# Performance work log

Hardware: AMD Instinct MI355X
Metric: run time of the kernel (lower is better)

The kernel has to match this reference:

```python
import jax, jax.numpy as jnp
import numpy as np
import math

D_MODEL, N_HEADS, D_HEAD, D_MLP = 768, 12, 64, 3072
LN_EPS = 1e-5
INIT_STD = 0.02


def gelu_new(x):
    # GPT-2 'new' gelu: 0.5*x*(1+tanh(sqrt(2/pi)*(x+0.044715*x^3)))
    c = math.sqrt(2.0 / math.pi)
    return 0.5 * x * (1.0 + jnp.tanh(c * (x + 0.044715 * jnp.power(x, 3.0))))


def layer_norm(x, w, b):
    mu = jnp.mean(x, axis=-1, keepdims=True)
    xc = x - mu
    scale = jnp.sqrt(jnp.mean(xc * xc, axis=-1, keepdims=True) + LN_EPS)
    return (xc / scale) * w + b


def setup_inputs() -> dict:
    key = jax.random.key(0)
    ks = jax.random.split(key, 8)
    resid_pre = jax.random.normal(ks[0], (8, 1024, D_MODEL), dtype=jnp.float32)
    W_Q = jax.random.normal(ks[1], (N_HEADS, D_MODEL, D_HEAD), dtype=jnp.float32) * INIT_STD
    W_K = jax.random.normal(ks[2], (N_HEADS, D_MODEL, D_HEAD), dtype=jnp.float32) * INIT_STD
    W_V = jax.random.normal(ks[3], (N_HEADS, D_MODEL, D_HEAD), dtype=jnp.float32) * INIT_STD
    W_O = jax.random.normal(ks[4], (N_HEADS, D_HEAD, D_MODEL), dtype=jnp.float32) * INIT_STD
    W_in = jax.random.normal(ks[5], (D_MODEL, D_MLP), dtype=jnp.float32) * INIT_STD
    W_out = jax.random.normal(ks[6], (D_MLP, D_MODEL), dtype=jnp.float32) * INIT_STD
    return {
        'resid_pre': resid_pre,
        'ln1_w': jnp.ones((D_MODEL,), jnp.float32), 'ln1_b': jnp.zeros((D_MODEL,), jnp.float32),
        'W_Q': W_Q, 'b_Q': jnp.zeros((N_HEADS, D_HEAD), jnp.float32),
        'W_K': W_K, 'b_K': jnp.zeros((N_HEADS, D_HEAD), jnp.float32),
        'W_V': W_V, 'b_V': jnp.zeros((N_HEADS, D_HEAD), jnp.float32),
        'W_O': W_O, 'b_O': jnp.zeros((D_MODEL,), jnp.float32),
        'ln2_w': jnp.ones((D_MODEL,), jnp.float32), 'ln2_b': jnp.zeros((D_MODEL,), jnp.float32),
        'W_in': W_in, 'b_in': jnp.zeros((D_MLP,), jnp.float32),
        'W_out': W_out, 'b_out': jnp.zeros((D_MODEL,), jnp.float32),
    }


def attention(x, W_Q, b_Q, W_K, b_K, W_V, b_V, W_O, b_O):
    # x: [b, s, d_model]
    q = jnp.einsum('bsd,hde->bshe', x, W_Q) + b_Q
    k = jnp.einsum('bsd,hde->bshe', x, W_K) + b_K
    v = jnp.einsum('bsd,hde->bshe', x, W_V) + b_V
    scores = jnp.einsum('bqhe,bkhe->bhqk', q, k) / math.sqrt(D_HEAD)
    s = x.shape[1]
    causal = jnp.triu(jnp.ones((s, s), dtype=bool), k=1)
    scores = jnp.where(causal, -jnp.inf, scores)
    pattern = jax.nn.softmax(scores, axis=-1)
    pattern = jnp.where(jnp.isnan(pattern), 0.0, pattern)
    z = jnp.einsum('bhqk,bkhe->bqhe', pattern, v)
    # per-head projection then sum over heads; b_O/n_heads per head sums to b_O
    return jnp.einsum('bqhe,hed->bqd', z, W_O) + b_O


def reference(resid_pre, ln1_w, ln1_b, W_Q, b_Q, W_K, b_K, W_V, b_V, W_O, b_O,
              ln2_w, ln2_b, W_in, b_in, W_out, b_out):
    normed1 = layer_norm(resid_pre, ln1_w, ln1_b)
    attn_out = attention(normed1, W_Q, b_Q, W_K, b_K, W_V, b_V, W_O, b_O)
    residual = resid_pre + attn_out
    normed2 = layer_norm(residual, ln2_w, ln2_b)
    pre = jnp.einsum('bsd,dm->bsm', normed2, W_in) + b_in
    mlp_out = jnp.einsum('bsm,md->bsd', gelu_new(pre), W_out) + b_out
    return residual + mlp_out
```

## Files before the change

kernel.cpp:

```cpp
#include <hip/hip_runtime.h>
#include <hip/hip_bf16.h>
#include <stdint.h>
#include <math.h>

typedef __bf16 bf16x8 __attribute__((ext_vector_type(8)));
typedef float f32x4 __attribute__((ext_vector_type(4)));
using bf16 = __hip_bfloat16;

__device__ inline float bf2f(bf16 x) { return __bfloat162float(x); }
__device__ inline bf16 f2bf(float x) { return __float2bfloat16(x); }

__device__ inline f32x4 mfma16(bf16x8 a, bf16x8 b, f32x4 c) {
  return __builtin_amdgcn_mfma_f32_16x16x32_bf16(a, b, c, 0, 0, 0);
}

__device__ inline void async16(const bf16* g, bf16* l) {
  __builtin_amdgcn_global_load_lds(
      (const __attribute__((address_space(1))) unsigned int*)g,
      (__attribute__((address_space(3))) unsigned int*)l, 16, 0, 0);
}

__device__ inline float gelu_new(float x) {
  float u2 = 1.5957691216057308f * (x + 0.044715f * x * x * x);
  float e = __expf(u2);
  float t = 1.0f - 2.0f * __builtin_amdgcn_rcpf(e + 1.0f);
  return 0.5f * x * (1.0f + t);
}

__device__ inline void ln_body(const float* __restrict__ x, const float* __restrict__ w,
                               const float* __restrict__ bb, bf16* __restrict__ out,
                               int row, int t, float* red) {
  size_t base = (size_t)row * 768;
  float v0 = x[base + t];
  float v1 = x[base + t + 256];
  float v2 = x[base + t + 512];
  float s = v0 + v1 + v2;
  float ss = v0 * v0 + v1 * v1 + v2 * v2;
#pragma unroll
  for (int off = 32; off > 0; off >>= 1) {
    s += __shfl_down(s, off, 64);
    ss += __shfl_down(ss, off, 64);
  }
  int wv = t >> 6, ln = t & 63;
  if (ln == 0) { red[wv] = s; red[4 + wv] = ss; }
  __syncthreads();
  s = red[0] + red[1] + red[2] + red[3];
  ss = red[4] + red[5] + red[6] + red[7];
  float mu = s * (1.0f / 768.0f);
  float var = ss * (1.0f / 768.0f) - mu * mu;
  float rinv = rsqrtf(var + 1e-5f);
  out[base + t]       = f2bf((v0 - mu) * rinv * w[t]       + bb[t]);
  out[base + t + 256] = f2bf((v1 - mu) * rinv * w[t + 256] + bb[t + 256]);
  out[base + t + 512] = f2bf((v2 - mu) * rinv * w[t + 512] + bb[t + 512]);
}

__global__ __launch_bounds__(256) void ln_kernel(const float* __restrict__ x,
                                                 const float* __restrict__ w,
                                                 const float* __restrict__ bb,
                                                 bf16* __restrict__ out) {
  __shared__ float red[8];
  ln_body(x, w, bb, out, blockIdx.x, threadIdx.x, red);
}

__device__ inline void transpose_body(const float* __restrict__ in, bf16* __restrict__ out,
                                      int R, int C, int bx, int by, int t,
                                      float (*tile)[33]) {
  int tx = t & 31, ty = t >> 5;
  int r0 = bx * 32, c0 = by * 32;
#pragma unroll
  for (int j = 0; j < 32; j += 8)
    tile[ty + j][tx] = in[(size_t)(r0 + ty + j) * C + c0 + tx];
  __syncthreads();
#pragma unroll
  for (int j = 0; j < 32; j += 8)
    out[(size_t)(c0 + ty + j) * R + r0 + tx] = f2bf(tile[tx][ty + j]);
}

__global__ __launch_bounds__(256) void prep_all(
    const float* __restrict__ resid_pre, const float* __restrict__ ln1_w,
    const float* __restrict__ ln1_b, bf16* __restrict__ n1,
    const float* __restrict__ Wq, const float* __restrict__ Wk,
    const float* __restrict__ Wv, bf16* __restrict__ Wqkv_t,
    const float* __restrict__ W_O, bf16* __restrict__ Wo_t,
    const float* __restrict__ W_in, bf16* __restrict__ Win_t,
    const float* __restrict__ W_out, bf16* __restrict__ Wout_t,
    const float* __restrict__ bq, const float* __restrict__ bk,
    const float* __restrict__ bv, float* __restrict__ bias_qkv) {
  __shared__ float tile[32][33];
  const int t = threadIdx.x;
  int bid = blockIdx.x;
  if (bid < 8192) {
    ln_body(resid_pre, ln1_w, ln1_b, n1, bid, t, &tile[0][0]);
    return;
  }
  bid -= 8192;
  if (bid < 1728) {
    int z = bid / 48, r = bid - z * 48;
    int which = z / 12, h = z - which * 12;
    const float* W = (which == 0) ? Wq : ((which == 1) ? Wk : Wv);
    transpose_body(W + (size_t)h * 768 * 64,
                   Wqkv_t + (size_t)which * 589824 + (size_t)h * 64 * 768,
                   768, 64, r % 24, r / 24, t, tile);
    return;
  }
  bid -= 1728;
  if (bid < 576) {
    transpose_body(W_O, Wo_t, 768, 768, bid % 24, bid / 24, t, tile);
    return;
  }
  bid -= 576;
  if (bid < 2304) {
    transpose_body(W_in, Win_t, 768, 3072, bid % 24, bid / 24, t, tile);
    return;
  }
  bid -= 2304;
  if (bid < 2304) {
    transpose_body(W_out, Wout_t, 3072, 768, bid % 96, bid / 96, t, tile);
    return;
  }
  bid -= 2304;
  int i = bid * 256 + t;
  if (i < 2304)
    bias_qkv[i] = (i < 768) ? bq[i] : ((i < 1536) ? bk[i - 768] : bv[i - 1536]);
}

enum { MODE_QKV = 0, MODE_ADDF = 2, MODE_GELU = 3 };

template <int MODE, int MROWS>
__global__ __launch_bounds__(256) void gemm_bt(
    const bf16* __restrict__ A, const bf16* __restrict__ BT,
    const float* __restrict__ bias,
    const float* __restrict__ addend,
    float* __restrict__ out_f32,
    bf16* __restrict__ out_bf16,
    int M, int N, int K) {
  constexpr int MI = MROWS / 32;
  __shared__ __align__(16) bf16 smem[(MROWS + 128) * 64];
  bf16* Alds = smem;
  bf16* Blds = smem + MROWS * 64;
  const int t = threadIdx.x;
  const int wave = t >> 6, lane = t & 63;
  const int lm = lane & 15, quad = lane >> 4;
  const int wm = wave >> 1, wn = wave & 1;
  const int m0 = blockIdx.x * MROWS, n0 = blockIdx.y * 128;

  f32x4 acc[MI][4] = {};

  for (int k0 = 0; k0 < K; k0 += 64) {
#pragma unroll
    for (int i = 0; i < MI; i++) {
      int c = i * 256 + t;
      int r = c >> 3, cs = c & 7;
      async16(A + (size_t)(m0 + r) * K + k0 + ((cs ^ (r & 7)) << 3), &Alds[c * 8]);
    }
#pragma unroll
    for (int i = 0; i < 4; i++) {
      int c = i * 256 + t;
      int r = c >> 3, cs = c & 7;
      async16(BT + (size_t)(n0 + r) * K + k0 + ((cs ^ (r & 7)) << 3), &Blds[c * 8]);
    }
    __syncthreads();
#pragma unroll
    for (int kk = 0; kk < 64; kk += 32) {
      const int cbase = kk >> 3;
      bf16x8 af[MI], bfr[4];
#pragma unroll
      for (int mi = 0; mi < MI; mi++)
        af[mi] = *(const bf16x8*)&Alds[(wm * (MROWS / 2) + mi * 16 + lm) * 64 +
                                       (((cbase + quad) ^ (lm & 7)) << 3)];
#pragma unroll
      for (int ni = 0; ni < 4; ni++)
        bfr[ni] = *(const bf16x8*)&Blds[(wn * 64 + ni * 16 + lm) * 64 +
                                        (((cbase + quad) ^ (lm & 7)) << 3)];
#pragma unroll
      for (int mi = 0; mi < MI; mi++)
#pragma unroll
        for (int ni = 0; ni < 4; ni++)
          acc[mi][ni] = mfma16(af[mi], bfr[ni], acc[mi][ni]);
    }
    __syncthreads();
  }

  float bv[4];
#pragma unroll
  for (int ni = 0; ni < 4; ni++) bv[ni] = bias[n0 + wn * 64 + ni * 16 + lm];

  float* sc = (float*)smem + wave * 1088;
  const bool vseg = (MODE == MODE_QKV) && ((n0 + wn * 64) >= 1536);

#pragma unroll
  for (int mi = 0; mi < MI; mi++) {
    __syncthreads();
#pragma unroll
    for (int ni = 0; ni < 4; ni++)
#pragma unroll
      for (int reg = 0; reg < 4; reg++) {
        float val = acc[mi][ni][reg] + bv[ni];
        if (vseg) sc[(ni * 16 + lm) * 17 + quad * 4 + reg] = val;
        else      sc[(quad * 4 + reg) * 67 + ni * 16 + lm] = val;
      }
    __syncthreads();

    if (!vseg) {
#pragma unroll
      for (int p = 0; p < 2; p++) {
        int rl = p * 8 + (lane >> 3);
        int cl = (lane & 7) * 8;
        float v[8];
#pragma unroll
        for (int j = 0; j < 8; j++) v[j] = sc[rl * 67 + cl + j];
        int rm = m0 + wm * (MROWS / 2) + mi * 16 + rl;
        int cn0 = n0 + wn * 64 + cl;
        if constexpr (MODE == MODE_GELU) {
          bf16x8 o;
#pragma unroll
          for (int j = 0; j < 8; j++) o[j] = (__bf16)gelu_new(v[j]);
          *(bf16x8*)(out_bf16 + (size_t)rm * N + cn0) = o;
        } else if constexpr (MODE == MODE_ADDF) {
          size_t idx = (size_t)rm * N + cn0;
          f32x4 a0 = *(const f32x4*)(addend + idx);
          f32x4 a1 = *(const f32x4*)(addend + idx + 4);
          f32x4 o0, o1;
#pragma unroll
          for (int j = 0; j < 4; j++) { o0[j] = v[j] + a0[j]; o1[j] = v[4 + j] + a1[j]; }
          *(f32x4*)(out_f32 + idx) = o0;
          *(f32x4*)(out_f32 + idx + 4) = o1;
        } else {
          int seg = cn0 / 768;
          int lnn = cn0 - seg * 768;
          int h2 = lnn >> 6, e0 = lnn & 63;
          int b2 = rm >> 10, sq = rm & 1023;
          float scale = (seg == 0) ? 0.125f : 1.0f;
          bf16x8 o;
#pragma unroll
          for (int j = 0; j < 8; j++) o[j] = (__bf16)(v[j] * scale);
          *(bf16x8*)(out_bf16 + (size_t)seg * 6291456 +
                     (((size_t)(b2 * 12 + h2) * 1024 + sq) << 6) + e0) = o;
        }
      }
    } else {
#pragma unroll
      for (int p = 0; p < 2; p++) {
        float v[8];
#pragma unroll
        for (int j = 0; j < 8; j++) v[j] = sc[lane * 17 + p * 8 + j];
        int e_he = n0 + wn * 64 + lane;
        int lnn = e_he - 1536;
        int h2 = lnn >> 6, e2 = lnn & 63;
        int s0 = m0 + wm * (MROWS / 2) + mi * 16 + p * 8;
        int b2 = s0 >> 10, sq = s0 & 1023;
        bf16x8 o;
#pragma unroll
        for (int j = 0; j < 8; j++) o[j] = (__bf16)v[j];
        *(bf16x8*)(out_bf16 + (size_t)2 * 6291456 +
                   (((size_t)(b2 * 12 + h2) * 64 + e2) << 10) + sq) = o;
      }
    }
  }
}

#define PHASE(BT_, AH, BH, STAGE, TAIL) do {                                          \
  bf16x8 af_[4][2], bf_[2][2];                                                        \
  _Pragma("unroll")                                                                   \
  for (int f_ = 0; f_ < 4; f_++) {                                                    \
    _Pragma("unroll")                                                                 \
    for (int k_ = 0; k_ < 2; k_++)                                                    \
      af_[f_][k_] = *(const bf16x8*)&sm[(BT_) * 32768 + (AH) * 8192 +                 \
                                        (aRow + f_ * 16) * 64 +                       \
                                        (((k_ * 4 + quad) ^ lms) << 3)];              \
  }                                                                                   \
  _Pragma("unroll")                                                                   \
  for (int g_ = 0; g_ < 2; g_++) {                                                    \
    _Pragma("unroll")                                                                 \
    for (int k_ = 0; k_ < 2; k_++)                                                    \
      bf_[g_][k_] = *(const bf16x8*)&sm[(BT_) * 32768 + 16384 + (BH) * 8192 +         \
                                        (bRow + g_ * 16) * 64 +                       \
                                        (((k_ * 4 + quad) ^ lms) << 3)];              \
  }                                                                                   \
  STAGE;                                                                              \
  __builtin_amdgcn_s_barrier();                                                       \
  __builtin_amdgcn_s_setprio(1);                                                      \
  _Pragma("unroll")                                                                   \
  for (int k_ = 0; k_ < 2; k_++) {                                                    \
    _Pragma("unroll")                                                                 \
    for (int f_ = 0; f_ < 4; f_++) {                                                  \
      _Pragma("unroll")                                                               \
      for (int g_ = 0; g_ < 2; g_++)                                                  \
        acc[AH][f_][BH][g_] = mfma16(af_[f_][k_], bf_[g_][k_], acc[AH][f_][BH][g_]);  \
    }                                                                                 \
  }                                                                                   \
  __builtin_amdgcn_s_setprio(0);                                                      \
  TAIL;                                                                               \
  __builtin_amdgcn_s_barrier();                                                       \
} while (0)

template <int MODE>
__global__ __launch_bounds__(512, 2) void gemm256(
    const bf16* __restrict__ A, const bf16* __restrict__ BT,
    const float* __restrict__ bias, bf16* __restrict__ out, int N) {
  __shared__ __align__(16) bf16 sm[65536];
  const int tid = threadIdx.x;
  const int wave = tid >> 6, lane = tid & 63;
  const int lm = lane & 15, quad = lane >> 4, lms = lm & 7;
  const int wm = wave >> 2, wn = wave & 3;

  const int cpx = gridDim.x >> 3;
  const int swz = (blockIdx.x & 7) * cpx + (blockIdx.x >> 3);
  const int m0 = (swz & 31) * 256;
  const int n0 = (swz >> 5) * 256;

  const int aRow = wm * 64 + lm;
  const int bRow = wn * 32 + lm;

  const int r0 = tid >> 3;
  const int of0 = (((tid & 7) ^ (r0 & 7)) << 3);
  const bf16* sA = A + (size_t)(m0 + r0) * 768 + of0;
  const bf16* sB = BT + (size_t)(n0 + r0) * 768 + of0;

  auto STA = [&](int bb, int ah, int t2) {
    bf16* d = sm + bb * 32768 + ah * 8192 + tid * 8;
    const bf16* s = sA + ah * 98304 + t2 * 64;
    async16(s, d);
    async16(s + 49152, d + 4096);
  };
  auto STB = [&](int bb, int bh, int t2) {
    bf16* d = sm + bb * 32768 + 16384 + bh * 8192 + tid * 8;
    const bf16* s = sB + bh * 98304 + t2 * 64;
    async16(s, d);
    async16(s + 49152, d + 4096);
  };

  f32x4 acc[2][4][2][2] = {};

  STA(0, 0, 0); STB(0, 0, 0); STA(0, 1, 0); STB(0, 1, 0);
  STA(1, 0, 1); STB(1, 0, 1);
  asm volatile("s_waitcnt vmcnt(4)" ::: "memory");
  __builtin_amdgcn_s_barrier();

#pragma unroll 2
  for (int tt = 0; tt < 12; ++tt) {
    const int bt = tt & 1;
    PHASE(bt, 0, 0, { if (tt + 1 < 12) STA(bt ^ 1, 1, tt + 1); }, {});
    PHASE(bt, 0, 1, { if (tt + 1 < 12) STB(bt ^ 1, 1, tt + 1); }, {});
    PHASE(bt, 1, 0, { if (tt + 2 < 12) STA(bt, 0, tt + 2); }, {});
    PHASE(bt, 1, 1, { if (tt + 2 < 12) STB(bt, 0, tt + 2); },
          {
            if (tt + 1 < 12) {
              if (tt + 2 < 12) asm volatile("s_waitcnt vmcnt(4)" ::: "memory");
              else             asm volatile("s_waitcnt vmcnt(0)" ::: "memory");
            }
          });
  }

  float bvv[2][2];
#pragma unroll
  for (int bh2 = 0; bh2 < 2; bh2++)
#pragma unroll
    for (int g = 0; g < 2; g++)
      bvv[bh2][g] = bias[n0 + bh2 * 128 + wn * 32 + g * 16 + lm];

  float* sc = (float*)sm + wave * 1088;

  if constexpr (MODE == MODE_GELU) {
#pragma unroll
    for (int mi = 0; mi < 8; mi++) {
      const int ah = mi >> 2, f = mi & 3;
#pragma unroll
      for (int bh2 = 0; bh2 < 2; bh2++)
#pragma unroll
        for (int g = 0; g < 2; g++)
#pragma unroll
          for (int reg = 0; reg < 4; reg++)
            sc[(quad * 4 + reg) * 68 + bh2 * 32 + g * 16 + lm] =
                acc[ah][f][bh2][g][reg] + bvv[bh2][g];
#pragma unroll
      for (int p = 0; p < 2; p++) {
        int slot = p * 64 + lane;
        int rw = slot >> 3, c8 = (slot & 7) * 8;
        f32x4 u0 = *(const f32x4*)&sc[rw * 68 + c8];
        f32x4 u1 = *(const f32x4*)&sc[rw * 68 + c8 + 4];
        int grow = m0 + ah * 128 + wm * 64 + f * 16 + rw;
        int bh3 = c8 >> 5, cc = c8 & 31;
        int gcol = n0 + bh3 * 128 + wn * 32 + cc;
        bf16x8 o;
#pragma unroll
        for (int j = 0; j < 4; j++) { o[j] = (__bf16)gelu_new(u0[j]); o[4 + j] = (__bf16)gelu_new(u1[j]); }
        *(bf16x8*)(out + (size_t)grow * N + gcol) = o;
      }
    }
  } else {
    const int seg = n0 / 768;
    const float scale = (seg == 0) ? 0.125f : 1.0f;
    if (seg < 2) {
      bf16* qout = out + (size_t)seg * 6291456;
#pragma unroll
      for (int mi = 0; mi < 8; mi++) {
        const int ah = mi >> 2, f = mi & 3;
#pragma unroll
        for (int bh2 = 0; bh2 < 2; bh2++)
#pragma unroll
          for (int g = 0; g < 2; g++)
#pragma unroll
            for (int reg = 0; reg < 4; reg++)
              sc[(quad * 4 + reg) * 68 + bh2 * 32 + g * 16 + lm] =
                  (acc[ah][f][bh2][g][reg] + bvv[bh2][g]) * scale;
#pragma unroll
        for (int p = 0; p < 2; p++) {
          int slot = p * 64 + lane;
          int rw = slot >> 3, c8 = (slot & 7) * 8;
          f32x4 u0 = *(const f32x4*)&sc[rw * 68 + c8];
          f32x4 u1 = *(const f32x4*)&sc[rw * 68 + c8 + 4];
          int grow = m0 + ah * 128 + wm * 64 + f * 16 + rw;
          int bh3 = c8 >> 5, cc = c8 & 31;
          int gcol = n0 + bh3 * 128 + wn * 32 + cc;
          int lnn = gcol - seg * 768;
          int h2 = lnn >> 6, e0 = lnn & 63;
          int b2 = grow >> 10, sq = grow & 1023;
          bf16x8 o;
#pragma unroll
          for (int j = 0; j < 4; j++) { o[j] = (__bf16)u0[j]; o[4 + j] = (__bf16)u1[j]; }
          *(bf16x8*)(qout + (((size_t)(b2 * 12 + h2) * 1024 + sq) << 6) + e0) = o;
        }
      }
    } else {
#pragma unroll
      for (int mi = 0; mi < 8; mi++) {
        const int ah = mi >> 2, f = mi & 3;
#pragma unroll
        for (int bh2 = 0; bh2 < 2; bh2++)
#pragma unroll
          for (int g = 0; g < 2; g++)
#pragma unroll
            for (int reg = 0; reg < 4; reg++)
              sc[(bh2 * 32 + g * 16 + lm) * 17 + quad * 4 + reg] =
                  acc[ah][f][bh2][g][reg] + bvv[bh2][g];
#pragma unroll
        for (int p = 0; p < 2; p++) {
          float v[8];
#pragma unroll
          for (int j = 0; j < 8; j++) v[j] = sc[lane * 17 + p * 8 + j];
          int bh3 = lane >> 5, cc = lane & 31;
          int gcol = n0 + bh3 * 128 + wn * 32 + cc;
          int lnn = gcol - 1536;
          int h2 = lnn >> 6, e2 = lnn & 63;
          int s0 = m0 + ah * 128 + wm * 64 + f * 16 + p * 8;
          int b2 = s0 >> 10, sq = s0 & 1023;
          bf16x8 o;
#pragma unroll
          for (int j = 0; j < 8; j++) o[j] = (__bf16)v[j];
          *(bf16x8*)(out + (size_t)2 * 6291456 +
                     (((size_t)(b2 * 12 + h2) * 64 + e2) << 10) + sq) = o;
        }
      }
    }
  }
}

__global__ __launch_bounds__(256) void attn_kernel(const bf16* __restrict__ q,
                                                   const bf16* __restrict__ k,
                                                   const bf16* __restrict__ vt,
                                                   bf16* __restrict__ z) {
  const int S = 1024, E = 64;
  __shared__ __align__(16) bf16 Klds[64 * 64];
  __shared__ __align__(16) bf16 Vlds[64 * 64];
  __shared__ __align__(16) bf16 Plds[4 * 16 * 64];
  const int pb = blockIdx.x;
  const int bh = blockIdx.y;
  const int t = threadIdx.x;
  const int wave = t >> 6, lane = t & 63;
  const int lm = lane & 15, quad = lane >> 4;
  const size_t bh_se = (size_t)bh * S * E;
  const int b = bh / 12, h = bh - b * 12;

  for (int seg = 0; seg < 2; seg++) {
    const int qt = seg ? (15 - pb) : pb;
    const int qrow = qt * 64 + wave * 16 + lm;
    bf16x8 qf0 = *(const bf16x8*)(q + bh_se + (size_t)qrow * E + quad * 8);
    bf16x8 qf1 = *(const bf16x8*)(q + bh_se + (size_t)qrow * E + 32 + quad * 8);

    f32x4 acco[4] = {};
    float lsum[4] = {0.f, 0.f, 0.f, 0.f};

    for (int kt = 0; kt <= qt; kt++) {
#pragma unroll
      for (int i = 0; i < 2; i++) {
        int c = i * 256 + t;
        int r = c >> 3, cs = c & 7;
        int sw = (cs ^ (r & 7)) << 3;
        async16(k + bh_se + (size_t)(kt * 64 + r) * E + sw, &Klds[c * 8]);
        async16(vt + bh_se + (size_t)r * S + kt * 64 + sw, &Vlds[c * 8]);
      }
      __syncthreads();

      f32x4 accs[4] = {};
#pragma unroll
      for (int ni = 0; ni < 4; ni++) {
        int row = ni * 16 + lm;
        bf16x8 kf0 = *(const bf16x8*)&Klds[row * 64 + ((quad ^ (lm & 7)) << 3)];
        bf16x8 kf1 = *(const bf16x8*)&Klds[row * 64 + (((4 + quad) ^ (lm & 7)) << 3)];
        accs[ni] = mfma16(qf0, kf0, accs[ni]);
        accs[ni] = mfma16(qf1, kf1, accs[ni]);
      }

      float pv[4][4];
      const int qg = wave * 16 + quad * 4;
      if (kt == qt) {
#pragma unroll
        for (int ni = 0; ni < 4; ni++)
#pragma unroll
          for (int reg = 0; reg < 4; reg++) {
            float e_ = __expf(accs[ni][reg]);
            pv[ni][reg] = ((ni * 16 + lm) > (qg + reg)) ? 0.f : e_;
          }
      } else {
#pragma unroll
        for (int ni = 0; ni < 4; ni++)
#pragma unroll
          for (int reg = 0; reg < 4; reg++)
            pv[ni][reg] = __expf(accs[ni][reg]);
      }

#pragma unroll
      for (int ni = 0; ni < 4; ni++)
#pragma unroll
        for (int reg = 0; reg < 4; reg++) {
          lsum[reg] += pv[ni][reg];
          int pr = quad * 4 + reg;
          int ce = ni * 16 + lm;
          Plds[wave * 1024 + pr * 64 + (((ce >> 3) ^ (pr & 7)) << 3) + (ce & 7)] =
              f2bf(pv[ni][reg]);
        }
      __syncthreads();

      bf16x8 pf0 = *(const bf16x8*)&Plds[wave * 1024 + lm * 64 + ((quad ^ (lm & 7)) << 3)];
      bf16x8 pf1 = *(const bf16x8*)&Plds[wave * 1024 + lm * 64 + (((4 + quad) ^ (lm & 7)) << 3)];
#pragma unroll
      for (int ni = 0; ni < 4; ni++) {
        int row = ni * 16 + lm;
        bf16x8 vf0 = *(const bf16x8*)&Vlds[row * 64 + ((quad ^ (lm & 7)) << 3)];
        bf16x8 vf1 = *(const bf16x8*)&Vlds[row * 64 + (((4 + quad) ^ (lm & 7)) << 3)];
        acco[ni] = mfma16(pf0, vf0, acco[ni]);
        acco[ni] = mfma16(pf1, vf1, acco[ni]);
      }
      __syncthreads();
    }

#pragma unroll
    for (int reg = 0; reg < 4; reg++) {
#pragma unroll
      for (int off = 1; off < 16; off <<= 1) lsum[reg] += __shfl_xor(lsum[reg], off, 16);
    }
    float rl[4];
#pragma unroll
    for (int reg = 0; reg < 4; reg++) rl[reg] = 1.0f / lsum[reg];

#pragma unroll
    for (int ni = 0; ni < 4; ni++)
#pragma unroll
      for (int reg = 0; reg < 4; reg++) {
        int srow = qt * 64 + wave * 16 + quad * 4 + reg;
        size_t idx = (((size_t)(b * 1024 + srow) * 12 + h) << 6) + ni * 16 + lm;
        z[idx] = f2bf(acco[ni][reg] * rl[reg]);
      }
  }
}

extern "C" void kernel_launch(void* const* d_in, const int* in_sizes, int n_in,
                              void* d_out, int out_size, void* d_ws, size_t ws_size,
                              hipStream_t stream) {
  (void)in_sizes; (void)n_in; (void)out_size; (void)ws_size;
  const float* resid_pre = (const float*)d_in[0];
  const float* ln1_w = (const float*)d_in[1];
  const float* ln1_b = (const float*)d_in[2];
  const float* W_Q = (const float*)d_in[3];
  const float* b_Q = (const float*)d_in[4];
  const float* W_K = (const float*)d_in[5];
  const float* b_K = (const float*)d_in[6];
  const float* W_V = (const float*)d_in[7];
  const float* b_V = (const float*)d_in[8];
  const float* W_O = (const float*)d_in[9];
  const float* b_O = (const float*)d_in[10];
  const float* ln2_w = (const float*)d_in[11];
  const float* ln2_b = (const float*)d_in[12];
  const float* W_in = (const float*)d_in[13];
  const float* b_in = (const float*)d_in[14];
  const float* W_out = (const float*)d_in[15];
  const float* b_out = (const float*)d_in[16];

  char* ws = (char*)d_ws;
  const size_t EB = (size_t)8192 * 768;
  bf16* n1     = (bf16*)(ws);
  bf16* qb     = (bf16*)(ws + EB * 2);
  bf16* zb     = (bf16*)(ws + EB * 8);
  float* resid = (float*)(ws + EB * 10);
  bf16* act    = (bf16*)(ws + EB * 2);
  char* wsw = ws + EB * 14;
  bf16* Wqkv_t = (bf16*)(wsw);
  bf16* Wo_t   = (bf16*)(wsw + 3 * 1179648);
  bf16* Win_t  = (bf16*)(wsw + 4 * 1179648);
  bf16* Wout_t = (bf16*)(wsw + 4 * 1179648 + 4718592);
  float* bias_qkv = (float*)(wsw + 4 * 1179648 + 4718592 + 9437184);
  bf16* kb  = qb + EB;
  bf16* vtb = qb + 2 * EB;

  prep_all<<<15113, 256, 0, stream>>>(resid_pre, ln1_w, ln1_b, n1,
                                      W_Q, W_K, W_V, Wqkv_t,
                                      W_O, Wo_t, W_in, Win_t, W_out, Wout_t,
                                      b_Q, b_K, b_V, bias_qkv);

  gemm256<MODE_QKV><<<288, 512, 0, stream>>>(n1, Wqkv_t, bias_qkv, qb, 2304);

  attn_kernel<<<dim3(8, 96), 256, 0, stream>>>(qb, kb, vtb, zb);

  gemm_bt<MODE_ADDF, 64><<<dim3(128, 6), 256, 0, stream>>>(
      zb, Wo_t, b_O, resid_pre, resid, nullptr, 8192, 768, 768);

  ln_kernel<<<8192, 256, 0, stream>>>(resid, ln2_w, ln2_b, n1);

  gemm256<MODE_GELU><<<384, 512, 0, stream>>>(n1, Win_t, b_in, act, 3072);

  gemm_bt<MODE_ADDF, 64><<<dim3(128, 6), 256, 0, stream>>>(
      act, Wout_t, b_out, resid, (float*)d_out, nullptr, 8192, 768, 3072);
}
```

Before: 364.5 us.

## Hold A/B fragments in registers and prefetch next halves during MFMA phases

Reworks the 256x256 GEMM main loop so A and B LDS fragments for both halves sit in persistent register arrays. The next half-tile is read from LDS one phase ahead of its use, and the first half of the next k-tile is read before the current tile finishes. This reuses fragments across phases instead of reloading them each phase. The aim is to hide LDS read latency behind MFMA work, at the cost of more registers under the 512x2 launch bounds, which could cause spills.

```diff
diff --git a/kernel.cpp b/kernel.cpp
--- a/kernel.cpp
+++ b/kernel.cpp
@@ -259,26 +259,29 @@
   }
 }
 
-#define PHASE(BT_, AH, BH, STAGE, TAIL) do {                                          \
-  bf16x8 af_[4][2], bf_[2][2];                                                        \
+#define READ_A(H, BUF) do {                                                           \
   _Pragma("unroll")                                                                   \
   for (int f_ = 0; f_ < 4; f_++) {                                                    \
     _Pragma("unroll")                                                                 \
     for (int k_ = 0; k_ < 2; k_++)                                                    \
-      af_[f_][k_] = *(const bf16x8*)&sm[(BT_) * 32768 + (AH) * 8192 +                 \
-                                        (aRow + f_ * 16) * 64 +                       \
-                                        (((k_ * 4 + quad) ^ lms) << 3)];              \
+      Af[H][f_][k_] = *(const bf16x8*)&sm[(BUF) * 32768 + (H) * 8192 +                \
+                                          (aRow + f_ * 16) * 64 +                     \
+                                          (((k_ * 4 + quad) ^ lms) << 3)];            \
   }                                                                                   \
+} while (0)
+
+#define READ_B(H, BUF) do {                                                           \
   _Pragma("unroll")                                                                   \
   for (int g_ = 0; g_ < 2; g_++) {                                                    \
     _Pragma("unroll")                                                                 \
     for (int k_ = 0; k_ < 2; k_++)                                                    \
-      bf_[g_][k_] = *(const bf16x8*)&sm[(BT_) * 32768 + 16384 + (BH) * 8192 +         \
-                                        (bRow + g_ * 16) * 64 +                       \
-                                        (((k_ * 4 + quad) ^ lms) << 3)];              \
+      Bf[H][g_][k_] = *(const bf16x8*)&sm[(BUF) * 32768 + 16384 + (H) * 8192 +        \
+                                          (bRow + g_ * 16) * 64 +                     \
+                                          (((k_ * 4 + quad) ^ lms) << 3)];            \
   }                                                                                   \
-  STAGE;                                                                              \
-  __builtin_amdgcn_s_barrier();                                                       \
+} while (0)
+
+#define DO_MFMA(AH, BH) do {                                                          \
   __builtin_amdgcn_s_setprio(1);                                                      \
   _Pragma("unroll")                                                                   \
   for (int k_ = 0; k_ < 2; k_++) {                                                    \
@@ -286,12 +289,11 @@
     for (int f_ = 0; f_ < 4; f_++) {                                                  \
       _Pragma("unroll")                                                               \
       for (int g_ = 0; g_ < 2; g_++)                                                  \
-        acc[AH][f_][BH][g_] = mfma16(af_[f_][k_], bf_[g_][k_], acc[AH][f_][BH][g_]);  \
+        acc[AH][f_][BH][g_] =                                                         \
+            mfma16(Af[AH][f_][k_], Bf[BH][g_][k_], acc[AH][f_][BH][g_]);              \
     }                                                                                 \
   }                                                                                   \
   __builtin_amdgcn_s_setprio(0);                                                      \
-  TAIL;                                                                               \
-  __builtin_amdgcn_s_barrier();                                                       \
 } while (0)
 
 template <int MODE>
@@ -331,25 +333,44 @@
   };
 
   f32x4 acc[2][4][2][2] = {};
+  bf16x8 Af[2][4][2];
+  bf16x8 Bf[2][2][2];
 
   STA(0, 0, 0); STB(0, 0, 0); STA(0, 1, 0); STB(0, 1, 0);
   STA(1, 0, 1); STB(1, 0, 1);
   asm volatile("s_waitcnt vmcnt(4)" ::: "memory");
   __builtin_amdgcn_s_barrier();
+  READ_A(0, 0);
+  READ_B(0, 0);
 
 #pragma unroll 2
   for (int tt = 0; tt < 12; ++tt) {
-    const int bt = tt & 1;
-    PHASE(bt, 0, 0, { if (tt + 1 < 12) STA(bt ^ 1, 1, tt + 1); }, {});
-    PHASE(bt, 0, 1, { if (tt + 1 < 12) STB(bt ^ 1, 1, tt + 1); }, {});
-    PHASE(bt, 1, 0, { if (tt + 2 < 12) STA(bt, 0, tt + 2); }, {});
-    PHASE(bt, 1, 1, { if (tt + 2 < 12) STB(bt, 0, tt + 2); },
-          {
-            if (tt + 1 < 12) {
-              if (tt + 2 < 12) asm volatile("s_waitcnt vmcnt(4)" ::: "memory");
-              else             asm volatile("s_waitcnt vmcnt(0)" ::: "memory");
-            }
-          });
+    const int c = tt & 1, nb = c ^ 1;
+    READ_B(1, c);
+    if (tt + 1 < 12) STA(nb, 1, tt + 1);
+    __builtin_amdgcn_s_barrier();
+    DO_MFMA(0, 0);
+    __builtin_amdgcn_s_barrier();
+    READ_A(1, c);
+    if (tt + 1 < 12) STB(nb, 1, tt + 1);
+    __builtin_amdgcn_s_barrier();
+    DO_MFMA(0, 1);
+    if (tt + 1 < 12) asm volatile("s_waitcnt vmcnt(4)" ::: "memory");
+    __builtin_amdgcn_s_barrier();
+    if (tt + 1 < 12) READ_A(0, nb);
+    if (tt + 2 < 12) STA(c, 0, tt + 2);
+    __builtin_amdgcn_s_barrier();
+    DO_MFMA(1, 0);
+    __builtin_amdgcn_s_barrier();
+    if (tt + 1 < 12) READ_B(0, nb);
+    if (tt + 2 < 12) STB(c, 0, tt + 2);
+    __builtin_amdgcn_s_barrier();
+    DO_MFMA(1, 1);
+    if (tt + 1 < 12) {
+      if (tt + 2 < 12) asm volatile("s_waitcnt vmcnt(4)" ::: "memory");
+      else             asm volatile("s_waitcnt vmcnt(0)" ::: "memory");
+    }
+    __builtin_amdgcn_s_barrier();
   }
 
   float bvv[2][2];
```

New measurement: 386.0 us. 1.06x slower.
